# Kernel tuning notes

Hardware: AMD Instinct MI355X
Metric: run time of the kernel (lower is better)

The kernel has to match this reference:

```python
import jax, jax.numpy as jnp
import numpy as np

HEADS = 16
HEAD_DIM = 64
NEG = 1000000000.0  # additive mask magnitude from source


def setup_inputs() -> dict:
    key = jax.random.key(0)
    ks = jax.random.split(key, 6)
    N, S, D = 4, 2048, 1024
    x = jax.random.normal(ks[0], (N, S, D), dtype=jnp.float32)
    scale = 1.0 / np.sqrt(D)
    wq = jax.random.normal(ks[1], (D, D), dtype=jnp.float32) * scale
    wk = jax.random.normal(ks[2], (D, D), dtype=jnp.float32) * scale
    wv = jax.random.normal(ks[3], (D, D), dtype=jnp.float32) * scale
    wo = jax.random.normal(ks[4], (D, D), dtype=jnp.float32) * scale
    bo = jnp.zeros((D,), dtype=jnp.float32)
    return {"x": x, "wq": wq, "wk": wk, "wv": wv, "wo": wo, "bo": bo}


def reference(x, wq, wk, wv, wo, bo):
    N, S, D = x.shape
    h, d = HEADS, HEAD_DIM
    attn_scale = 1.0 / np.sqrt(d)
    # projections (no bias, qkv_bias=False)
    q = (x @ wq.T).reshape(N, S, h, d).transpose(0, 2, 1, 3)  # N h S d
    k = (x @ wk.T).reshape(N, S, h, d).transpose(0, 2, 1, 3)  # N h S d
    v = (x @ wv.T).reshape(N, S, h, d).transpose(0, 2, 1, 3)  # N h S d
    logits = jnp.einsum('nhsd,nhtd->nhst', q, k) * attn_scale  # N h S S
    scores = jax.nn.softmax(logits, axis=-1)
    # faithful quirk: additive mask applied AFTER softmax
    # triu(ones) - 1 -> 0 on/above diagonal, -1 strictly below
    causal_mask = NEG * (jnp.triu(jnp.ones((S, S), dtype=x.dtype)) - 1.0)
    scores = scores + causal_mask  # broadcasts over N, h
    out = jnp.einsum('nhst,nhtd->nhsd', scores, v)  # N h S d
    out = out.transpose(0, 2, 1, 3).reshape(N, S, h * d)
    return out @ wo.T + bo  # dropout p=0 -> identity
```

## Files before the change

kernel.cpp:

```cpp
#include <hip/hip_runtime.h>

#define AS1 __attribute__((address_space(1)))
#define AS3 __attribute__((address_space(3)))

typedef __bf16 bf16x8 __attribute__((ext_vector_type(8)));
typedef float f32x4 __attribute__((ext_vector_type(4)));

__device__ __forceinline__ unsigned short f2bf(float f) {
  unsigned int u = __float_as_uint(f);
  return (unsigned short)((u + 0x7fffu + ((u >> 16) & 1u)) >> 16);
}

__device__ __forceinline__ void gemm_body(int bx, int by, int bz,
                                          const unsigned short* __restrict__ A,
                                          const unsigned short* __restrict__ B,
                                          float* __restrict__ C,
                                          const float* __restrict__ bias,
                                          int ldC, int K, int kchunk, int planeElems,
                                          unsigned short* lA, unsigned short* lB) {
  int tid = threadIdx.x;
  int w = tid >> 6, lane = tid & 63;
  int r0 = bx * 128, c0 = by * 128;
  int wr = w >> 1, wc = w & 1;
  int ml = lane & 15, q = lane >> 4;
  C += (size_t)bz * planeElems;

  int srow = lane >> 3;
  int scol = 8 * ((lane & 7) ^ srow);
  const unsigned short* gA = A + (size_t)(r0 + 32 * w + srow) * K + scol + (size_t)bz * kchunk;
  const unsigned short* gB = B + (size_t)(c0 + 32 * w + srow) * K + scol + (size_t)bz * kchunk;
  unsigned short* lApw = lA + 32 * w * 64;
  unsigned short* lBpw = lB + 32 * w * 64;

  const f32x4 vzero = {0.f, 0.f, 0.f, 0.f};
  f32x4 acc[4][4];
#pragma unroll
  for (int mt = 0; mt < 4; ++mt)
#pragma unroll
    for (int nt = 0; nt < 4; ++nt) acc[mt][nt] = vzero;

  for (int k0 = 0; k0 < kchunk; k0 += 64) {
#pragma unroll
    for (int n = 0; n < 4; ++n) {
      __builtin_amdgcn_global_load_lds((const AS1 void*)(gA + (size_t)8 * n * K + k0),
                                       (AS3 void*)(lApw + n * 512), 16, 0, 0);
      __builtin_amdgcn_global_load_lds((const AS1 void*)(gB + (size_t)8 * n * K + k0),
                                       (AS3 void*)(lBpw + n * 512), 16, 0, 0);
    }
    __syncthreads();
#pragma unroll
    for (int h = 0; h < 2; ++h) {
      bf16x8 af[4], bfv[4];
      int kb = 4 * h + q;
#pragma unroll
      for (int mt = 0; mt < 4; ++mt) {
        int R = 64 * wr + 16 * mt + ml;
        af[mt] = *(const bf16x8*)(lA + R * 64 + 8 * (kb ^ (ml & 7)));
      }
#pragma unroll
      for (int nt = 0; nt < 4; ++nt) {
        int R = 64 * wc + 16 * nt + ml;
        bfv[nt] = *(const bf16x8*)(lB + R * 64 + 8 * (kb ^ (ml & 7)));
      }
#pragma unroll
      for (int mt = 0; mt < 4; ++mt)
#pragma unroll
        for (int nt = 0; nt < 4; ++nt)
          acc[mt][nt] = __builtin_amdgcn_mfma_f32_16x16x32_bf16(af[mt], bfv[nt], acc[mt][nt], 0, 0, 0);
    }
    __syncthreads();
  }

#pragma unroll
  for (int nt = 0; nt < 4; ++nt) {
    int col = c0 + 64 * wc + 16 * nt + ml;
    float bv = bias ? bias[col] : 0.f;
#pragma unroll
    for (int mt = 0; mt < 4; ++mt) {
      int rowb = r0 + 64 * wr + 16 * mt + q * 4;
#pragma unroll
      for (int r = 0; r < 4; ++r)
        C[(size_t)(rowb + r) * ldC + col] = acc[mt][nt][r] + bv;
    }
  }
}

__global__ __launch_bounds__(256) void prep_tilesum_k(const float* __restrict__ x,
                                                      const float* __restrict__ wo,
                                                      const float* __restrict__ wv,
                                                      float* __restrict__ T,
                                                      unsigned short* __restrict__ wo_b,
                                                      unsigned short* __restrict__ wvT_b) {
  __shared__ float t[32][33];
  int b = blockIdx.x;
  if (b < 256) {
    int bt = b >> 1;
    int f = (b & 1) * 512 + threadIdx.x * 2;
    const float* p = x + (size_t)bt * 65536 + f;
    float sx = 0.f, sy = 0.f;
#pragma unroll 8
    for (int i = 0; i < 64; ++i) {
      float2 v = *(const float2*)(p + (size_t)i * 1024);
      sx += v.x; sy += v.y;
    }
    float2 s = {sx, sy};
    *(float2*)(T + (size_t)bt * 1024 + f) = s;
  } else if (b < 1280) {
    int i = ((b - 256) * 256 + threadIdx.x) * 4;
    float4 v = *(const float4*)(wo + i);
    ushort4 o;
    o.x = f2bf(v.x); o.y = f2bf(v.y); o.z = f2bf(v.z); o.w = f2bf(v.w);
    *(ushort4*)(wo_b + i) = o;
  } else {
    int bb = b - 1280;
    int bx = (bb & 31) * 32, by = (bb >> 5) * 32;
    int tx = threadIdx.x & 31, ty = threadIdx.x >> 5;
    for (int i = ty; i < 32; i += 8) t[i][tx] = wv[(by + i) * 1024 + bx + tx];
    __syncthreads();
    for (int i = ty; i < 32; i += 8) wvT_b[(bx + i) * 1024 + by + tx] = f2bf(t[tx][i]);
  }
}

__global__ __launch_bounds__(256) void scan_smallgemm_k(const float* __restrict__ x,
                                                        const float* __restrict__ T,
                                                        unsigned short* __restrict__ Xc,
                                                        const unsigned short* __restrict__ wo_b,
                                                        const unsigned short* __restrict__ wvT_b,
                                                        float* __restrict__ Pf) {
  __shared__ unsigned short lA[128 * 64];
  __shared__ unsigned short lB[128 * 64];
  int b = blockIdx.x;
  if (b < 256) {
    int g = b;
    gemm_body(g & 7, (g >> 3) & 7, g >> 6, wo_b, wvT_b, Pf, nullptr,
              1024, 1024, 256, 1 << 20, lA, lB);
  } else {
    int sb = b - 256;
    int bt = sb >> 1;
    int tile = bt & 31, b0 = bt - tile;
    int f = (sb & 1) * 512 + threadIdx.x * 2;
    float ax = 0.f, ay = 0.f;
    for (int t = 0; t < tile; ++t) {
      float2 v = *(const float2*)(T + (size_t)(b0 + t) * 1024 + f);
      ax += v.x; ay += v.y;
    }
    const float* px = x + (size_t)bt * 65536 + f;
    unsigned short* po = Xc + (size_t)bt * 65536 + f;
#pragma unroll 4
    for (int i = 0; i < 64; ++i) {
      unsigned int pk = (unsigned int)f2bf(ax) | ((unsigned int)f2bf(ay) << 16);
      *(unsigned int*)(po + (size_t)i * 1024) = pk;
      float2 v = *(const float2*)(px + (size_t)i * 1024);
      ax += v.x; ay += v.y;
    }
  }
}

__global__ __launch_bounds__(256) void reduce_cast_k(const float* __restrict__ P,
                                                     unsigned short* __restrict__ Mp) {
  int i = (blockIdx.x * 256 + threadIdx.x) * 4;
  float4 a = *(const float4*)(P + i);
  float4 b = *(const float4*)(P + (1u << 20) + i);
  float4 c = *(const float4*)(P + (2u << 20) + i);
  float4 d = *(const float4*)(P + (3u << 20) + i);
  ushort4 o;
  o.x = f2bf(-1e9f * (a.x + b.x + c.x + d.x));
  o.y = f2bf(-1e9f * (a.y + b.y + c.y + d.y));
  o.z = f2bf(-1e9f * (a.z + b.z + c.z + d.z));
  o.w = f2bf(-1e9f * (a.w + b.w + c.w + d.w));
  *(ushort4*)(Mp + i) = o;
}

__global__ __launch_bounds__(256) void gemm_big_k(const unsigned short* __restrict__ A,
                                                  const unsigned short* __restrict__ B,
                                                  float* __restrict__ C,
                                                  const float* __restrict__ bias) {
  __shared__ unsigned short lA[128 * 64];
  __shared__ unsigned short lB[128 * 64];
  int p = blockIdx.x;
  int l = (p & 7) * 64 + (p >> 3);
  gemm_body(l >> 3, l & 7, 0, A, B, C, bias, 1024, 1024, 1024, 0, lA, lB);
}

extern "C" void kernel_launch(void* const* d_in, const int* in_sizes, int n_in,
                              void* d_out, int out_size, void* d_ws, size_t ws_size,
                              hipStream_t stream) {
  const float* x  = (const float*)d_in[0];
  const float* wv = (const float*)d_in[3];
  const float* wo = (const float*)d_in[4];
  const float* bo = (const float*)d_in[5];
  char* ws = (char*)d_ws;

  unsigned short* wo_b  = (unsigned short*)ws;
  unsigned short* wvT_b = (unsigned short*)(ws + (2u << 20));
  unsigned short* Mp    = (unsigned short*)(ws + (4u << 20));
  float*          Tsum  = (float*)(ws + (6u << 20));
  unsigned short* Xc    = (unsigned short*)(ws + (7u << 20));
  float*          Pf    = (float*)(ws + (23u << 20));

  prep_tilesum_k<<<2304, 256, 0, stream>>>(x, wo, wv, Tsum, wo_b, wvT_b);
  scan_smallgemm_k<<<512, 256, 0, stream>>>(x, Tsum, Xc, wo_b, wvT_b, Pf);
  reduce_cast_k<<<1024, 256, 0, stream>>>(Pf, Mp);
  gemm_big_k<<<512, 256, 0, stream>>>(Xc, Mp, (float*)d_out, bo);
}
```

Baseline: 143.7 us.

## Drop split-K reduce kernel, fuse mask scale and bf16 cast into small GEMM epilogue

The small wo·wvT GEMM no longer splits K across four planes followed by a separate reduce/cast kernel. Each of 64 blocks now runs the full K=1024 and writes the -1e9-scaled bf16 result directly, which removes one launch and the fp32 partial-plane traffic. The tile-sum and prefix-scan paths are also widened to float4 per thread with half as many blocks. The cost is far fewer blocks for the small GEMM (64 instead of 256), so it has less parallelism and a longer serial K loop, though it shares the launch with the 128 scan blocks.

```diff
diff --git a/kernel.cpp b/kernel.cpp
--- a/kernel.cpp
+++ b/kernel.cpp
@@ -15,6 +15,7 @@
                                           const unsigned short* __restrict__ A,
                                           const unsigned short* __restrict__ B,
                                           float* __restrict__ C,
+                                          unsigned short* __restrict__ Cb,
                                           const float* __restrict__ bias,
                                           int ldC, int K, int kchunk, int planeElems,
                                           unsigned short* lA, unsigned short* lB) {
@@ -23,7 +24,6 @@
   int r0 = bx * 128, c0 = by * 128;
   int wr = w >> 1, wc = w & 1;
   int ml = lane & 15, q = lane >> 4;
-  C += (size_t)bz * planeElems;
 
   int srow = lane >> 3;
   int scol = 8 * ((lane & 7) ^ srow);
@@ -71,16 +71,31 @@
     __syncthreads();
   }
 
-#pragma unroll
-  for (int nt = 0; nt < 4; ++nt) {
-    int col = c0 + 64 * wc + 16 * nt + ml;
-    float bv = bias ? bias[col] : 0.f;
-#pragma unroll
-    for (int mt = 0; mt < 4; ++mt) {
-      int rowb = r0 + 64 * wr + 16 * mt + q * 4;
-#pragma unroll
-      for (int r = 0; r < 4; ++r)
-        C[(size_t)(rowb + r) * ldC + col] = acc[mt][nt][r] + bv;
+  if (Cb) {
+#pragma unroll
+    for (int nt = 0; nt < 4; ++nt) {
+      int col = c0 + 64 * wc + 16 * nt + ml;
+#pragma unroll
+      for (int mt = 0; mt < 4; ++mt) {
+        int rowb = r0 + 64 * wr + 16 * mt + q * 4;
+#pragma unroll
+        for (int r = 0; r < 4; ++r)
+          Cb[(size_t)(rowb + r) * ldC + col] = f2bf(-1e9f * acc[mt][nt][r]);
+      }
+    }
+  } else {
+    C += (size_t)bz * planeElems;
+#pragma unroll
+    for (int nt = 0; nt < 4; ++nt) {
+      int col = c0 + 64 * wc + 16 * nt + ml;
+      float bv = bias ? bias[col] : 0.f;
+#pragma unroll
+      for (int mt = 0; mt < 4; ++mt) {
+        int rowb = r0 + 64 * wr + 16 * mt + q * 4;
+#pragma unroll
+        for (int r = 0; r < 4; ++r)
+          C[(size_t)(rowb + r) * ldC + col] = acc[mt][nt][r] + bv;
+      }
     }
   }
 }
@@ -93,26 +108,25 @@
                                                       unsigned short* __restrict__ wvT_b) {
   __shared__ float t[32][33];
   int b = blockIdx.x;
-  if (b < 256) {
-    int bt = b >> 1;
-    int f = (b & 1) * 512 + threadIdx.x * 2;
-    const float* p = x + (size_t)bt * 65536 + f;
-    float sx = 0.f, sy = 0.f;
+  if (b < 128) {
+    int f = threadIdx.x * 4;
+    const float* p = x + (size_t)b * 65536 + f;
+    float sx = 0.f, sy = 0.f, sz = 0.f, sw = 0.f;
 #pragma unroll 8
     for (int i = 0; i < 64; ++i) {
-      float2 v = *(const float2*)(p + (size_t)i * 1024);
-      sx += v.x; sy += v.y;
-    }
-    float2 s = {sx, sy};
-    *(float2*)(T + (size_t)bt * 1024 + f) = s;
-  } else if (b < 1280) {
-    int i = ((b - 256) * 256 + threadIdx.x) * 4;
+      float4 v = *(const float4*)(p + (size_t)i * 1024);
+      sx += v.x; sy += v.y; sz += v.z; sw += v.w;
+    }
+    float4 s = {sx, sy, sz, sw};
+    *(float4*)(T + (size_t)b * 1024 + f) = s;
+  } else if (b < 1152) {
+    int i = ((b - 128) * 256 + threadIdx.x) * 4;
     float4 v = *(const float4*)(wo + i);
     ushort4 o;
     o.x = f2bf(v.x); o.y = f2bf(v.y); o.z = f2bf(v.z); o.w = f2bf(v.w);
     *(ushort4*)(wo_b + i) = o;
   } else {
-    int bb = b - 1280;
+    int bb = b - 1152;
     int bx = (bb & 31) * 32, by = (bb >> 5) * 32;
     int tx = threadIdx.x & 31, ty = threadIdx.x >> 5;
     for (int i = ty; i < 32; i += 8) t[i][tx] = wv[(by + i) * 1024 + bx + tx];
@@ -126,49 +140,35 @@
                                                         unsigned short* __restrict__ Xc,
                                                         const unsigned short* __restrict__ wo_b,
                                                         const unsigned short* __restrict__ wvT_b,
-                                                        float* __restrict__ Pf) {
+                                                        unsigned short* __restrict__ Mp) {
   __shared__ unsigned short lA[128 * 64];
   __shared__ unsigned short lB[128 * 64];
   int b = blockIdx.x;
-  if (b < 256) {
-    int g = b;
-    gemm_body(g & 7, (g >> 3) & 7, g >> 6, wo_b, wvT_b, Pf, nullptr,
-              1024, 1024, 256, 1 << 20, lA, lB);
+  if (b < 64) {
+    gemm_body(b & 7, b >> 3, 0, wo_b, wvT_b, nullptr, Mp, nullptr,
+              1024, 1024, 1024, 0, lA, lB);
   } else {
-    int sb = b - 256;
-    int bt = sb >> 1;
+    int bt = b - 64;
     int tile = bt & 31, b0 = bt - tile;
-    int f = (sb & 1) * 512 + threadIdx.x * 2;
-    float ax = 0.f, ay = 0.f;
-    for (int t = 0; t < tile; ++t) {
-      float2 v = *(const float2*)(T + (size_t)(b0 + t) * 1024 + f);
-      ax += v.x; ay += v.y;
+    int f = threadIdx.x * 4;
+    float ax = 0.f, ay = 0.f, az = 0.f, aw = 0.f;
+#pragma unroll 4
+    for (int t2 = 0; t2 < tile; ++t2) {
+      float4 v = *(const float4*)(T + (size_t)(b0 + t2) * 1024 + f);
+      ax += v.x; ay += v.y; az += v.z; aw += v.w;
     }
     const float* px = x + (size_t)bt * 65536 + f;
     unsigned short* po = Xc + (size_t)bt * 65536 + f;
 #pragma unroll 4
     for (int i = 0; i < 64; ++i) {
-      unsigned int pk = (unsigned int)f2bf(ax) | ((unsigned int)f2bf(ay) << 16);
-      *(unsigned int*)(po + (size_t)i * 1024) = pk;
-      float2 v = *(const float2*)(px + (size_t)i * 1024);
-      ax += v.x; ay += v.y;
-    }
-  }
-}
-
-__global__ __launch_bounds__(256) void reduce_cast_k(const float* __restrict__ P,
-                                                     unsigned short* __restrict__ Mp) {
-  int i = (blockIdx.x * 256 + threadIdx.x) * 4;
-  float4 a = *(const float4*)(P + i);
-  float4 b = *(const float4*)(P + (1u << 20) + i);
-  float4 c = *(const float4*)(P + (2u << 20) + i);
-  float4 d = *(const float4*)(P + (3u << 20) + i);
-  ushort4 o;
-  o.x = f2bf(-1e9f * (a.x + b.x + c.x + d.x));
-  o.y = f2bf(-1e9f * (a.y + b.y + c.y + d.y));
-  o.z = f2bf(-1e9f * (a.z + b.z + c.z + d.z));
-  o.w = f2bf(-1e9f * (a.w + b.w + c.w + d.w));
-  *(ushort4*)(Mp + i) = o;
+      uint2 pk;
+      pk.x = (unsigned int)f2bf(ax) | ((unsigned int)f2bf(ay) << 16);
+      pk.y = (unsigned int)f2bf(az) | ((unsigned int)f2bf(aw) << 16);
+      *(uint2*)(po + (size_t)i * 1024) = pk;
+      float4 v = *(const float4*)(px + (size_t)i * 1024);
+      ax += v.x; ay += v.y; az += v.z; aw += v.w;
+    }
+  }
 }
 
 __global__ __launch_bounds__(256) void gemm_big_k(const unsigned short* __restrict__ A,
@@ -179,7 +179,8 @@
   __shared__ unsigned short lB[128 * 64];
   int p = blockIdx.x;
   int l = (p & 7) * 64 + (p >> 3);
-  gemm_body(l >> 3, l & 7, 0, A, B, C, bias, 1024, 1024, 1024, 0, lA, lB);
+  gemm_body(l >> 3, l & 7, 0, A, B, C, nullptr, bias,
+            1024, 1024, 1024, 0, lA, lB);
 }
 
 extern "C" void kernel_launch(void* const* d_in, const int* in_sizes, int n_in,
@@ -196,10 +197,8 @@
   unsigned short* Mp    = (unsigned short*)(ws + (4u << 20));
   float*          Tsum  = (float*)(ws + (6u << 20));
   unsigned short* Xc    = (unsigned short*)(ws + (7u << 20));
-  float*          Pf    = (float*)(ws + (23u << 20));
-
-  prep_tilesum_k<<<2304, 256, 0, stream>>>(x, wo, wv, Tsum, wo_b, wvT_b);
-  scan_smallgemm_k<<<512, 256, 0, stream>>>(x, Tsum, Xc, wo_b, wvT_b, Pf);
-  reduce_cast_k<<<1024, 256, 0, stream>>>(Pf, Mp);
+
+  prep_tilesum_k<<<2176, 256, 0, stream>>>(x, wo, wv, Tsum, wo_b, wvT_b);
+  scan_smallgemm_k<<<192, 256, 0, stream>>>(x, Tsum, Xc, wo_b, wvT_b, Mp);
   gemm_big_k<<<512, 256, 0, stream>>>(Xc, Mp, (float*)d_out, bo);
 }
```

After: 139.9 us, median of 2. 2.7% less time.
